# Optimization experiments

Measured on AMD Instinct MI355X. Metric: run time of the kernel, lower is better.

The kernel has to match this reference:

```python
import jax, jax.numpy as jnp
import numpy as np

QMAX = 127.0
QMIN = -128.0


def setup_inputs() -> dict:
    key = jax.random.key(0)
    k1, k2, k3 = jax.random.split(key, 3)
    B, N, D, O = 4, 4096, 2048, 2048
    x = jax.random.normal(k1, (B, N, D), dtype=jnp.float32)
    weight = jax.random.normal(k2, (O, D), dtype=jnp.float32)
    bias = jax.random.normal(k3, (O,), dtype=jnp.float32)
    return {"x": x, "weight": weight, "bias": bias}


def reference(x, weight, bias):
    # --- per-row symmetric int8 quantization of the weight [O, D] ---
    w_max = jnp.clip(jnp.max(jnp.abs(weight), axis=1, keepdims=True), 1e-8, None)
    w_scale = (w_max / QMAX)                     # [O, 1]
    w_q = jnp.clip(jnp.round(weight / w_scale), QMIN, QMAX).astype(jnp.int8)
    w_scale = w_scale.squeeze(1).astype(jnp.float32)  # [O]

    # --- dynamic per-row symmetric int8 quantization of x [B, N, D] ---
    x_max = jnp.max(jnp.abs(x), axis=2, keepdims=True)       # [B, N, 1]
    x_scale = jnp.maximum(x_max / QMAX, 1e-12)               # [B, N, 1]
    x_q = jnp.clip(jnp.round(x / x_scale), QMIN, QMAX).astype(jnp.int8)

    # --- int8 GEMM accumulated in int32: [B,N,D] x [O,D]^T -> [B,N,O] ---
    acc = jnp.einsum("bnd,od->bno", x_q.astype(jnp.int32), w_q.astype(jnp.int32))

    # --- dequantize with per-row activation scale and per-out-channel weight scale ---
    y = acc.astype(jnp.float32) * x_scale.astype(jnp.float32) * w_scale[None, None, :]
    y = y + bias
    return y.astype(x.dtype)
```

## Files before the change

kernel.cpp:

```cpp
#include <hip/hip_runtime.h>
#include <stdint.h>
#include <stddef.h>

typedef int v4i __attribute__((ext_vector_type(4)));

#define GLOAD_LDS16(g, l) __builtin_amdgcn_global_load_lds( \
    (const __attribute__((address_space(1))) void*)(g),     \
    (__attribute__((address_space(3))) void*)(l), 16, 0, 0)

__device__ __forceinline__ int pack4(float4 f, float s) {
    int a = (int)rintf(f.x / s); a = a < -128 ? -128 : (a > 127 ? 127 : a);
    int b = (int)rintf(f.y / s); b = b < -128 ? -128 : (b > 127 ? 127 : b);
    int c = (int)rintf(f.z / s); c = c < -128 ? -128 : (c > 127 ? 127 : c);
    int d = (int)rintf(f.w / s); d = d < -128 ? -128 : (d > 127 ? 127 : d);
    return (a & 255) | ((b & 255) << 8) | ((c & 255) << 16) | ((d & 255) << 24);
}

__global__ __launch_bounds__(256) void quant_rows_2048(
    const float* __restrict__ in, signed char* __restrict__ q,
    float* __restrict__ scales, float floorv)
{
    const int lane = threadIdx.x & 63;
    const int row  = blockIdx.x * 4 + (threadIdx.x >> 6);
    const float* rp = in + (size_t)row * 2048;

    float4 v[8];
#pragma unroll
    for (int j = 0; j < 2; ++j) {
        const float4* p = (const float4*)(rp + j * 1024 + lane * 16);
#pragma unroll
        for (int i = 0; i < 4; ++i) v[j * 4 + i] = p[i];
    }
    float am = 0.0f;
#pragma unroll
    for (int i = 0; i < 8; ++i) {
        am = fmaxf(am, fabsf(v[i].x));
        am = fmaxf(am, fabsf(v[i].y));
        am = fmaxf(am, fabsf(v[i].z));
        am = fmaxf(am, fabsf(v[i].w));
    }
#pragma unroll
    for (int off = 32; off; off >>= 1) am = fmaxf(am, __shfl_xor(am, off));
    const float s = fmaxf(am / 127.0f, floorv);

#pragma unroll
    for (int j = 0; j < 2; ++j) {
        int4 pk;
        pk.x = pack4(v[j * 4 + 0], s);
        pk.y = pack4(v[j * 4 + 1], s);
        pk.z = pack4(v[j * 4 + 2], s);
        pk.w = pack4(v[j * 4 + 3], s);
        *(int4*)(q + (size_t)row * 2048 + j * 1024 + lane * 16) = pk;
    }
    if (lane == 0) scales[row] = s;
}

__global__ __launch_bounds__(256) void gemm_i8(
    const signed char* __restrict__ xq, const signed char* __restrict__ wq,
    const float* __restrict__ xs, const float* __restrict__ ws,
    const float* __restrict__ bias, float* __restrict__ out, int K)
{
    __shared__ __align__(16) signed char ldsA[128 * 128];
    __shared__ __align__(16) signed char ldsB[128 * 128];

    const int tid  = threadIdx.x;
    const int lane = tid & 63;
    const int wid  = tid >> 6;
    const int wm   = wid >> 1;
    const int wn   = wid & 1;
    const int brow = blockIdx.y * 128;
    const int bcol = blockIdx.x * 128;

    v4i acc[4][4] = {};

    const int r_sub  = tid >> 3;
    const int chunk  = tid & 7;
    const int nkt    = K >> 7;

    for (int kt = 0; kt < nkt; ++kt) {
        const size_t kbase = (size_t)kt * 128;
#pragma unroll
        for (int c = 0; c < 4; ++c) {
            const int r = c * 32 + r_sub;
            const int g = chunk ^ (r & 7);
            GLOAD_LDS16(xq + (size_t)(brow + r) * K + kbase + g * 16,
                        &ldsA[r * 128 + chunk * 16]);
        }
#pragma unroll
        for (int c = 0; c < 4; ++c) {
            const int r = c * 32 + r_sub;
            const int g = chunk ^ (r & 7);
            GLOAD_LDS16(wq + (size_t)(bcol + r) * K + kbase + g * 16,
                        &ldsB[r * 128 + chunk * 16]);
        }
        __syncthreads();

        const int ko = lane >> 4;
        const int rl = lane & 15;
#pragma unroll
        for (int kk = 0; kk < 2; ++kk) {
            v4i af[4], bf[4];
#pragma unroll
            for (int m = 0; m < 4; ++m) {
                const int row = wm * 64 + m * 16 + rl;
                const int sc  = (kk * 4 + ko) ^ (row & 7);
                af[m] = *(const v4i*)&ldsA[row * 128 + sc * 16];
            }
#pragma unroll
            for (int n = 0; n < 4; ++n) {
                const int row = wn * 64 + n * 16 + rl;
                const int sc  = (kk * 4 + ko) ^ (row & 7);
                bf[n] = *(const v4i*)&ldsB[row * 128 + sc * 16];
            }
#pragma unroll
            for (int m = 0; m < 4; ++m)
#pragma unroll
                for (int n = 0; n < 4; ++n)
                    acc[m][n] = __builtin_amdgcn_mfma_i32_16x16x64_i8(
                        af[m], bf[n], acc[m][n], 0, 0, 0);
        }
        __syncthreads();
    }

    const int rl = lane & 15;
    const int rg = lane >> 4;
#pragma unroll
    for (int n = 0; n < 4; ++n) {
        const int col = bcol + wn * 64 + n * 16 + rl;
        const float wsc = ws[col];
        const float bv  = bias[col];
#pragma unroll
        for (int m = 0; m < 4; ++m) {
#pragma unroll
            for (int j = 0; j < 4; ++j) {
                const int row = brow + wm * 64 + m * 16 + rg * 4 + j;
                out[(size_t)row * 2048 + col] =
                    (float)acc[m][n][j] * xs[row] * wsc + bv;
            }
        }
    }
}

extern "C" void kernel_launch(void* const* d_in, const int* in_sizes, int n_in,
                              void* d_out, int out_size, void* d_ws, size_t ws_size,
                              hipStream_t stream) {
    const float* x    = (const float*)d_in[0];
    const float* w    = (const float*)d_in[1];
    const float* bias = (const float*)d_in[2];
    float* out = (float*)d_out;

    const int D = 2048;
    const int O = in_sizes[2];
    const int M = in_sizes[0] / D;

    char* wsb = (char*)d_ws;
    signed char* xq = (signed char*)wsb;
    signed char* wqp = (signed char*)(wsb + (size_t)M * D);
    float* xs  = (float*)(wsb + (size_t)M * D + (size_t)O * D);
    float* wsc = (float*)(wsb + (size_t)M * D + (size_t)O * D + (size_t)M * 4);

    quant_rows_2048<<<M / 4, 256, 0, stream>>>(x, xq, xs, 1e-12f);
    quant_rows_2048<<<O / 4, 256, 0, stream>>>(w, wqp, wsc, 1e-8f / 127.0f);

    dim3 grid(O / 128, M / 128);
    gemm_i8<<<grid, 256, 0, stream>>>(xq, wqp, xs, wsc, bias, out, D);
}
```

Before: 138.7 us.

## Pipeline int8 GEMM with 4-stage LDS ring, 256x256 tiles and block swizzle

Replaces the single-buffered 128x128 GEMM with a 256x256 tile per 512-thread block that uses a 4-deep ring of 64-wide K slices in LDS (128 KB). Global-to-LDS loads for tile t+3 are issued in pieces between MFMA groups, with explicit vmcnt waits, barriers and setprio around MFMA bursts. Block indices are swizzled for L2 locality. This aims to hide memory latency and raise data reuse per tile. In exchange it uses much more LDS, which limits occupancy, and relies on hand-placed waitcnt timing whose correctness is fragile.

Measured after the change: 126.0 us. 1.1x faster.

```diff
diff --git a/kernel.cpp b/kernel.cpp
--- a/kernel.cpp
+++ b/kernel.cpp
@@ -55,74 +55,116 @@
     if (lane == 0) scales[row] = s;
 }
 
-__global__ __launch_bounds__(256) void gemm_i8(
+__global__ __launch_bounds__(512, 2) void gemm_i8_pipe(
     const signed char* __restrict__ xq, const signed char* __restrict__ wq,
     const float* __restrict__ xs, const float* __restrict__ ws,
     const float* __restrict__ bias, float* __restrict__ out, int K)
 {
-    __shared__ __align__(16) signed char ldsA[128 * 128];
-    __shared__ __align__(16) signed char ldsB[128 * 128];
+    __shared__ __align__(16) signed char lds[131072];
 
     const int tid  = threadIdx.x;
     const int lane = tid & 63;
     const int wid  = tid >> 6;
-    const int wm   = wid >> 1;
-    const int wn   = wid & 1;
-    const int brow = blockIdx.y * 128;
-    const int bcol = blockIdx.x * 128;
-
-    v4i acc[4][4] = {};
-
-    const int r_sub  = tid >> 3;
-    const int chunk  = tid & 7;
-    const int nkt    = K >> 7;
-
-    for (int kt = 0; kt < nkt; ++kt) {
-        const size_t kbase = (size_t)kt * 128;
-#pragma unroll
-        for (int c = 0; c < 4; ++c) {
-            const int r = c * 32 + r_sub;
-            const int g = chunk ^ (r & 7);
-            GLOAD_LDS16(xq + (size_t)(brow + r) * K + kbase + g * 16,
-                        &ldsA[r * 128 + chunk * 16]);
-        }
-#pragma unroll
-        for (int c = 0; c < 4; ++c) {
-            const int r = c * 32 + r_sub;
-            const int g = chunk ^ (r & 7);
-            GLOAD_LDS16(wq + (size_t)(bcol + r) * K + kbase + g * 16,
-                        &ldsB[r * 128 + chunk * 16]);
-        }
-        __syncthreads();
-
-        const int ko = lane >> 4;
-        const int rl = lane & 15;
-#pragma unroll
-        for (int kk = 0; kk < 2; ++kk) {
-            v4i af[4], bf[4];
-#pragma unroll
-            for (int m = 0; m < 4; ++m) {
-                const int row = wm * 64 + m * 16 + rl;
-                const int sc  = (kk * 4 + ko) ^ (row & 7);
-                af[m] = *(const v4i*)&ldsA[row * 128 + sc * 16];
-            }
-#pragma unroll
-            for (int n = 0; n < 4; ++n) {
-                const int row = wn * 64 + n * 16 + rl;
-                const int sc  = (kk * 4 + ko) ^ (row & 7);
-                bf[n] = *(const v4i*)&ldsB[row * 128 + sc * 16];
-            }
-#pragma unroll
-            for (int m = 0; m < 4; ++m)
-#pragma unroll
-                for (int n = 0; n < 4; ++n)
-                    acc[m][n] = __builtin_amdgcn_mfma_i32_16x16x64_i8(
-                        af[m], bf[n], acc[m][n], 0, 0, 0);
-        }
-        __syncthreads();
-    }
-
-    const int rl = lane & 15;
+    const int wm   = wid >> 2;
+    const int wn   = wid & 3;
+
+    const int nwg  = gridDim.x * gridDim.y;
+    int orig = blockIdx.y * gridDim.x + blockIdx.x;
+    int swz  = ((nwg & 7) == 0) ? ((orig & 7) * (nwg >> 3) + (orig >> 3)) : orig;
+    const int brow = (swz / gridDim.x) * 256;
+    const int bcol = (swz % gridDim.x) * 256;
+
+    const int srow = tid >> 2;
+    const int gch  = (((tid & 3) ^ ((tid >> 3) & 3)) << 4);
+    const int lofs = tid << 4;
+    const signed char* gA = xq + (size_t)(brow + srow) * K;
+    const signed char* gB = wq + (size_t)(bcol + srow) * K;
+
+#define ST_A(tt, half) GLOAD_LDS16(gA + (size_t)(half) * 128 * K + (size_t)(tt) * 64 + gch, \
+                                   lds + ((((tt) & 3) << 14) + ((half) << 13) + lofs))
+#define ST_B(tt, half) GLOAD_LDS16(gB + (size_t)(half) * 128 * K + (size_t)(tt) * 64 + gch, \
+                                   lds + (65536 + (((tt) & 3) << 14) + ((half) << 13) + lofs))
+
+    const int rl   = lane & 15;
+    const int ko   = lane >> 4;
+    const int slot = ((ko ^ ((rl >> 1) & 3)) << 4);
+
+#define FRAG_A(buf, r) (*(const v4i*)(lds + (((buf) << 14) + (r) * 64 + slot)))
+#define FRAG_B(buf, r) (*(const v4i*)(lds + (65536 + ((buf) << 14) + (r) * 64 + slot)))
+
+    v4i acc[8][4] = {};
+
+#define MFMA8(M0, M1)                                                              \
+    do {                                                                           \
+        __builtin_amdgcn_s_setprio(1);                                             \
+        acc[M0][0] = __builtin_amdgcn_mfma_i32_16x16x64_i8(a0, bf0, acc[M0][0], 0, 0, 0); \
+        acc[M0][1] = __builtin_amdgcn_mfma_i32_16x16x64_i8(a0, bf1, acc[M0][1], 0, 0, 0); \
+        acc[M0][2] = __builtin_amdgcn_mfma_i32_16x16x64_i8(a0, bf2, acc[M0][2], 0, 0, 0); \
+        acc[M0][3] = __builtin_amdgcn_mfma_i32_16x16x64_i8(a0, bf3, acc[M0][3], 0, 0, 0); \
+        acc[M1][0] = __builtin_amdgcn_mfma_i32_16x16x64_i8(a1, bf0, acc[M1][0], 0, 0, 0); \
+        acc[M1][1] = __builtin_amdgcn_mfma_i32_16x16x64_i8(a1, bf1, acc[M1][1], 0, 0, 0); \
+        acc[M1][2] = __builtin_amdgcn_mfma_i32_16x16x64_i8(a1, bf2, acc[M1][2], 0, 0, 0); \
+        acc[M1][3] = __builtin_amdgcn_mfma_i32_16x16x64_i8(a1, bf3, acc[M1][3], 0, 0, 0); \
+        __builtin_amdgcn_s_setprio(0);                                             \
+    } while (0)
+
+#define BAR()  __builtin_amdgcn_s_barrier()
+#define LGKM0() asm volatile("s_waitcnt lgkmcnt(0)" ::: "memory")
+
+    auto tile = [&](int t, bool issue) {
+        const int buf = t & 3;
+        const int ar  = wm * 128 + rl;
+        const int br  = wn * 64 + rl;
+        v4i bf0 = FRAG_B(buf, br);
+        v4i bf1 = FRAG_B(buf, br + 16);
+        v4i bf2 = FRAG_B(buf, br + 32);
+        v4i bf3 = FRAG_B(buf, br + 48);
+        v4i a0  = FRAG_A(buf, ar);
+        v4i a1  = FRAG_A(buf, ar + 16);
+        if (issue) ST_A(t + 3, 0);
+        BAR(); LGKM0();
+        MFMA8(0, 1);
+        BAR();
+        a0 = FRAG_A(buf, ar + 32);
+        a1 = FRAG_A(buf, ar + 48);
+        if (issue) ST_A(t + 3, 1);
+        BAR(); LGKM0();
+        MFMA8(2, 3);
+        BAR();
+        a0 = FRAG_A(buf, ar + 64);
+        a1 = FRAG_A(buf, ar + 80);
+        if (issue) ST_B(t + 3, 0);
+        BAR(); LGKM0();
+        MFMA8(4, 5);
+        BAR();
+        a0 = FRAG_A(buf, ar + 96);
+        a1 = FRAG_A(buf, ar + 112);
+        if (issue) ST_B(t + 3, 1);
+        BAR(); LGKM0();
+        MFMA8(6, 7);
+    };
+
+    ST_A(0, 0); ST_A(0, 1); ST_B(0, 0); ST_B(0, 1);
+    ST_A(1, 0); ST_A(1, 1); ST_B(1, 0); ST_B(1, 1);
+    ST_A(2, 0); ST_A(2, 1); ST_B(2, 0); ST_B(2, 1);
+    asm volatile("s_waitcnt vmcnt(8)" ::: "memory");
+    BAR();
+
+    const int NT = K >> 6;
+    int t = 0;
+    for (; t < NT - 3; ++t) {
+        tile(t, true);
+        asm volatile("s_waitcnt vmcnt(8)" ::: "memory");
+        BAR();
+    }
+    tile(NT - 3, false);
+    asm volatile("s_waitcnt vmcnt(4)" ::: "memory");
+    BAR();
+    tile(NT - 2, false);
+    asm volatile("s_waitcnt vmcnt(0)" ::: "memory");
+    BAR();
+    tile(NT - 1, false);
+
     const int rg = lane >> 4;
 #pragma unroll
     for (int n = 0; n < 4; ++n) {
@@ -130,15 +172,22 @@
         const float wsc = ws[col];
         const float bv  = bias[col];
 #pragma unroll
-        for (int m = 0; m < 4; ++m) {
+        for (int m = 0; m < 8; ++m) {
 #pragma unroll
             for (int j = 0; j < 4; ++j) {
-                const int row = brow + wm * 64 + m * 16 + rg * 4 + j;
+                const int row = brow + wm * 128 + m * 16 + rg * 4 + j;
                 out[(size_t)row * 2048 + col] =
                     (float)acc[m][n][j] * xs[row] * wsc + bv;
             }
         }
     }
+#undef ST_A
+#undef ST_B
+#undef FRAG_A
+#undef FRAG_B
+#undef MFMA8
+#undef BAR
+#undef LGKM0
 }
 
 extern "C" void kernel_launch(void* const* d_in, const int* in_sizes, int n_in,
@@ -154,7 +203,7 @@
     const int M = in_sizes[0] / D;
 
     char* wsb = (char*)d_ws;
-    signed char* xq = (signed char*)wsb;
+    signed char* xq  = (signed char*)wsb;
     signed char* wqp = (signed char*)(wsb + (size_t)M * D);
     float* xs  = (float*)(wsb + (size_t)M * D + (size_t)O * D);
     float* wsc = (float*)(wsb + (size_t)M * D + (size_t)O * D + (size_t)M * 4);
@@ -162,6 +211,6 @@
     quant_rows_2048<<<M / 4, 256, 0, stream>>>(x, xq, xs, 1e-12f);
     quant_rows_2048<<<O / 4, 256, 0, stream>>>(w, wqp, wsc, 1e-8f / 127.0f);
 
-    dim3 grid(O / 128, M / 128);
-    gemm_i8<<<grid, 256, 0, stream>>>(xq, wqp, xs, wsc, bias, out, D);
-}
+    dim3 grid(O / 256, M / 256);
+    gemm_i8_pipe<<<grid, 512, 0, stream>>>(xq, wqp, xs, wsc, bias, out, D);
+}
```

## Double-buffer LDS in int8 GEMM with 128x256 tiles, 512 threads, and tile swizzle

Applied to the files above, without the earlier changes.

Restructures the int8 GEMM to use 128x256 output tiles with 8 waves per block and a K-step of 64. Shared memory is double-buffered so the global-to-LDS loads for the next K slice are issued before the MFMAs on the current one, leaving one barrier per iteration. It also adds a block-index swizzle to improve L2 reuse and a new XOR swizzle for 64-byte LDS rows. The aim is to hide global load latency and raise occupancy, at the cost of more barriers in total, a smaller K per barrier, and 48KB of LDS per block.

New measurement: 126.4 us. 8.8% less time.

```diff
diff --git a/kernel.cpp b/kernel.cpp
--- a/kernel.cpp
+++ b/kernel.cpp
@@ -55,74 +55,71 @@
     if (lane == 0) scales[row] = s;
 }
 
-__global__ __launch_bounds__(256) void gemm_i8(
+__global__ __launch_bounds__(512, 4) void gemm_i8_occ(
     const signed char* __restrict__ xq, const signed char* __restrict__ wq,
     const float* __restrict__ xs, const float* __restrict__ ws,
     const float* __restrict__ bias, float* __restrict__ out, int K)
 {
-    __shared__ __align__(16) signed char ldsA[128 * 128];
-    __shared__ __align__(16) signed char ldsB[128 * 128];
+    __shared__ __align__(16) signed char lds[49152];
 
     const int tid  = threadIdx.x;
     const int lane = tid & 63;
     const int wid  = tid >> 6;
-    const int wm   = wid >> 1;
-    const int wn   = wid & 1;
-    const int brow = blockIdx.y * 128;
-    const int bcol = blockIdx.x * 128;
+    const int wm   = wid >> 2;
+    const int wn   = wid & 3;
+
+    const int nwg  = gridDim.x * gridDim.y;
+    int orig = blockIdx.y * gridDim.x + blockIdx.x;
+    int swz  = ((nwg & 7) == 0) ? ((orig & 7) * (nwg >> 3) + (orig >> 3)) : orig;
+    const int brow = (swz / gridDim.x) * 128;
+    const int bcol = (swz % gridDim.x) * 256;
+
+    const int gch  = (((tid & 3) ^ ((tid >> 3) & 3)) << 4);
+    const int lofs = tid << 4;
+    const signed char* gA  = xq + (size_t)(brow + (tid >> 2)) * K;
+    const signed char* gB0 = wq + (size_t)(bcol + (tid >> 2)) * K;
+    const signed char* gB1 = wq + (size_t)(bcol + 128 + (tid >> 2)) * K;
+
+#define ST_A(tt, bb)  GLOAD_LDS16(gA  + (size_t)(tt) * 64 + gch, lds + ((bb) ? 8192 : 0) + lofs)
+#define ST_B0(tt, bb) GLOAD_LDS16(gB0 + (size_t)(tt) * 64 + gch, lds + 16384 + ((bb) ? 16384 : 0) + lofs)
+#define ST_B1(tt, bb) GLOAD_LDS16(gB1 + (size_t)(tt) * 64 + gch, lds + 24576 + ((bb) ? 16384 : 0) + lofs)
+
+    const int rl   = lane & 15;
+    const int ko   = lane >> 4;
+    const int slot = ((ko ^ ((rl >> 1) & 3)) << 4);
+
+#define FRAG_A(bb, r) (*(const v4i*)(lds + (((bb) ? 8192 : 0) + (r) * 64 + slot)))
+#define FRAG_B(bb, r) (*(const v4i*)(lds + (16384 + ((bb) ? 16384 : 0) + (r) * 64 + slot)))
 
     v4i acc[4][4] = {};
+    const int ar = wm * 64 + rl;
+    const int br = wn * 64 + rl;
 
-    const int r_sub  = tid >> 3;
-    const int chunk  = tid & 7;
-    const int nkt    = K >> 7;
+    ST_A(0, 0); ST_B0(0, 0); ST_B1(0, 0);
+    __syncthreads();
 
-    for (int kt = 0; kt < nkt; ++kt) {
-        const size_t kbase = (size_t)kt * 128;
+    const int NT = K >> 6;
+    for (int t = 0; t < NT; ++t) {
+        const int buf = t & 1;
+        if (t + 1 < NT) {
+            ST_A(t + 1, buf ^ 1);
+            ST_B0(t + 1, buf ^ 1);
+            ST_B1(t + 1, buf ^ 1);
+        }
+        v4i af[4], bf[4];
 #pragma unroll
-        for (int c = 0; c < 4; ++c) {
-            const int r = c * 32 + r_sub;
-            const int g = chunk ^ (r & 7);
-            GLOAD_LDS16(xq + (size_t)(brow + r) * K + kbase + g * 16,
-                        &ldsA[r * 128 + chunk * 16]);
-        }
+        for (int m = 0; m < 4; ++m) af[m] = FRAG_A(buf, ar + m * 16);
 #pragma unroll
-        for (int c = 0; c < 4; ++c) {
-            const int r = c * 32 + r_sub;
-            const int g = chunk ^ (r & 7);
-            GLOAD_LDS16(wq + (size_t)(bcol + r) * K + kbase + g * 16,
-                        &ldsB[r * 128 + chunk * 16]);
-        }
-        __syncthreads();
-
-        const int ko = lane >> 4;
-        const int rl = lane & 15;
+        for (int n = 0; n < 4; ++n) bf[n] = FRAG_B(buf, br + n * 16);
 #pragma unroll
-        for (int kk = 0; kk < 2; ++kk) {
-            v4i af[4], bf[4];
+        for (int m = 0; m < 4; ++m)
 #pragma unroll
-            for (int m = 0; m < 4; ++m) {
-                const int row = wm * 64 + m * 16 + rl;
-                const int sc  = (kk * 4 + ko) ^ (row & 7);
-                af[m] = *(const v4i*)&ldsA[row * 128 + sc * 16];
-            }
-#pragma unroll
-            for (int n = 0; n < 4; ++n) {
-                const int row = wn * 64 + n * 16 + rl;
-                const int sc  = (kk * 4 + ko) ^ (row & 7);
-                bf[n] = *(const v4i*)&ldsB[row * 128 + sc * 16];
-            }
-#pragma unroll
-            for (int m = 0; m < 4; ++m)
-#pragma unroll
-                for (int n = 0; n < 4; ++n)
-                    acc[m][n] = __builtin_amdgcn_mfma_i32_16x16x64_i8(
-                        af[m], bf[n], acc[m][n], 0, 0, 0);
-        }
+            for (int n = 0; n < 4; ++n)
+                acc[m][n] = __builtin_amdgcn_mfma_i32_16x16x64_i8(
+                    af[m], bf[n], acc[m][n], 0, 0, 0);
         __syncthreads();
     }
 
-    const int rl = lane & 15;
     const int rg = lane >> 4;
 #pragma unroll
     for (int n = 0; n < 4; ++n) {
@@ -139,6 +136,11 @@
             }
         }
     }
+#undef ST_A
+#undef ST_B0
+#undef ST_B1
+#undef FRAG_A
+#undef FRAG_B
 }
 
 extern "C" void kernel_launch(void* const* d_in, const int* in_sizes, int n_in,
@@ -154,7 +156,7 @@
     const int M = in_sizes[0] / D;
 
     char* wsb = (char*)d_ws;
-    signed char* xq = (signed char*)wsb;
+    signed char* xq  = (signed char*)wsb;
     signed char* wqp = (signed char*)(wsb + (size_t)M * D);
     float* xs  = (float*)(wsb + (size_t)M * D + (size_t)O * D);
     float* wsc = (float*)(wsb + (size_t)M * D + (size_t)O * D + (size_t)M * 4);
@@ -162,6 +164,6 @@
     quant_rows_2048<<<M / 4, 256, 0, stream>>>(x, xq, xs, 1e-12f);
     quant_rows_2048<<<O / 4, 256, 0, stream>>>(w, wqp, wsc, 1e-8f / 127.0f);
 
-    dim3 grid(O / 128, M / 128);
-    gemm_i8<<<grid, 256, 0, stream>>>(xq, wqp, xs, wsc, bias, out, D);
+    dim3 grid(O / 256, M / 128);
+    gemm_i8_occ<<<grid, 512, 0, stream>>>(xq, wqp, xs, wsc, bias, out, D);
 }
```
